# Kernel optimization log

Hardware: AMD Instinct MI355X
Metric: run time of the kernel (lower is better)

Reference implementation:

```python
import jax, jax.numpy as jnp
from jax import lax
import numpy as np

I, H, C = 128, 512, 1000  # input_dim, hidden_dim, num_classes
B, S = 256, 512           # batch, seq_len


def setup_inputs() -> dict:
    key = jax.random.key(0)
    ks = jax.random.split(key, 7)
    k = 1.0 / np.sqrt(H)  # pytorch GRU/Linear init range
    return {
        "x": jax.random.normal(ks[0], (B, S, I), dtype=jnp.float32),
        "W_ih": jax.random.uniform(ks[1], (3 * H, I), minval=-k, maxval=k, dtype=jnp.float32),
        "W_hh": jax.random.uniform(ks[2], (3 * H, H), minval=-k, maxval=k, dtype=jnp.float32),
        "b_ih": jax.random.uniform(ks[3], (3 * H,), minval=-k, maxval=k, dtype=jnp.float32),
        "b_hh": jax.random.uniform(ks[4], (3 * H,), minval=-k, maxval=k, dtype=jnp.float32),
        "W_head": jax.random.uniform(ks[5], (C, H), minval=-k, maxval=k, dtype=jnp.float32),
        "b_head": jax.random.uniform(ks[6], (C,), minval=-k, maxval=k, dtype=jnp.float32),
    }


def reference(x, W_ih, W_hh, b_ih, b_hh, W_head, b_head):
    # Precompute input projections for all timesteps: [B,S,3H] -> [S,B,3H]
    x_gates = jnp.einsum("bsi,gi->bsg", x, W_ih) + b_ih
    x_gates = jnp.transpose(x_gates, (1, 0, 2))

    h0 = jnp.zeros((x.shape[0], W_hh.shape[1]), dtype=x.dtype)

    def step(h, xg):
        hg = h @ W_hh.T + b_hh  # [B,3H]
        xr, xz, xn = jnp.split(xg, 3, axis=-1)
        hr, hz, hn = jnp.split(hg, 3, axis=-1)
        r = jax.nn.sigmoid(xr + hr)
        z = jax.nn.sigmoid(xz + hz)
        n = jnp.tanh(xn + r * hn)
        h_new = (1.0 - z) * n + z * h
        return h_new, None

    hT, _ = lax.scan(step, h0, x_gates)  # final hidden state == outputs[:, -1, :]
    return hT @ W_head.T + b_head  # [B, C]
```

## Files before the change

kernel.cpp:

```cpp
#include <hip/hip_runtime.h>


#define NB 256
#define NH 512
#define NI 128
#define NC 1000
#define NS 512

typedef __attribute__((ext_vector_type(8))) short bf16x8;
typedef __attribute__((ext_vector_type(4))) float f32x4;

__device__ __forceinline__ unsigned short f2bf(float f) {
    unsigned u = __builtin_bit_cast(unsigned, f);
    return (unsigned short)((u + 0x7FFFu + ((u >> 16) & 1u)) >> 16);
}

__device__ __forceinline__ bf16x8 pack8(const float* v) {
    bf16x8 r;
#pragma unroll
    for (int i = 0; i < 8; ++i) r[i] = (short)f2bf(v[i]);
    return r;
}

__device__ __forceinline__ unsigned long long ld_agent_u64(const unsigned long long* p) {
    return __hip_atomic_load(p, __ATOMIC_RELAXED, __HIP_MEMORY_SCOPE_AGENT);
}
__device__ __forceinline__ unsigned int ld_agent_u32(const unsigned int* p) {
    return __hip_atomic_load(p, __ATOMIC_RELAXED, __HIP_MEMORY_SCOPE_AGENT);
}
__device__ __forceinline__ void st_agent_u16(unsigned short* p, unsigned short v) {
    __hip_atomic_store(p, v, __ATOMIC_RELAXED, __HIP_MEMORY_SCOPE_AGENT);
}
__device__ __forceinline__ void st_agent_u32(unsigned int* p, unsigned int v) {
    __hip_atomic_store(p, v, __ATOMIC_RELAXED, __HIP_MEMORY_SCOPE_AGENT);
}

__global__ void gru_init_ws(unsigned int* __restrict__ fl) {
    const int i = blockIdx.x * 256 + threadIdx.x;
    if (i < 512) fl[i] = 0u;
}

__global__ void __launch_bounds__(256, 1) gru_scan(
    const float* __restrict__ x,
    const float* __restrict__ Wih,
    const float* __restrict__ Whh,
    const float* __restrict__ bih,
    const float* __restrict__ bhh,
    unsigned short* __restrict__ hbuf,
    float* __restrict__ hT,
    unsigned int* __restrict__ flags)
{
    const int tid = threadIdx.x;
    const int l   = tid & 63;
    const int w   = tid >> 6;
    const int ch  = w & 1;
    const int kh  = w >> 1;
    const int bid = blockIdx.x;
    const int g   = bid & 15;
    const int jb  = bid >> 4;
    const int r0  = g << 4;
    const int cw0 = (jb << 5) + (ch << 4);
    const int l15 = l & 15;
    const int lq  = l >> 4;
    const int c_col = cw0 + l15;

    __shared__ float part[4][4][64][4];

    bf16x8 whh[3][8];
#pragma unroll
    for (int gt = 0; gt < 3; ++gt) {
        const float* wr = Whh + (size_t)(gt * NH + c_col) * NH;
#pragma unroll
        for (int ks = 0; ks < 8; ++ks) {
            const int k0 = kh * 256 + ks * 32 + lq * 8;
            float tmp[8];
            *(f32x4*)(tmp)     = *(const f32x4*)(wr + k0);
            *(f32x4*)(tmp + 4) = *(const f32x4*)(wr + k0 + 4);
            whh[gt][ks] = pack8(tmp);
        }
    }
    bf16x8 wih[3][2];
#pragma unroll
    for (int gt = 0; gt < 3; ++gt) {
        const float* wr = Wih + (size_t)(gt * NH + c_col) * NI;
#pragma unroll
        for (int ks = 0; ks < 2; ++ks) {
            const int k0 = kh * 64 + ks * 32 + lq * 8;
            float tmp[8];
            *(f32x4*)(tmp)     = *(const f32x4*)(wr + k0);
            *(f32x4*)(tmp + 4) = *(const f32x4*)(wr + k0 + 4);
            wih[gt][ks] = pack8(tmp);
        }
    }

    float bR = bih[c_col] + bhh[c_col];
    float bZ = bih[NH + c_col] + bhh[NH + c_col];
    float bNx = bih[2 * NH + c_col];
    float bNh = bhh[2 * NH + c_col];
    if (kh != 0) { bR = bZ = bNx = bNh = 0.f; }

    float hold0 = 0.f, hold1 = 0.f;

    const float* xptr0 = x + (size_t)(r0 + l15) * (NS * NI) + kh * 64 + lq * 8;
    unsigned int* fl = flags + g * 32;

    const int lanep8 = ((ch * 2 + (l15 >> 3)) * 16 + lq * 4 + kh * 2) * 8;
    const int est    = l15 & 7;

    f32x4 xp0 = *(const f32x4*)(xptr0 + 0);
    f32x4 xp1 = *(const f32x4*)(xptr0 + 4);
    f32x4 xp2 = *(const f32x4*)(xptr0 + 32);
    f32x4 xp3 = *(const f32x4*)(xptr0 + 36);

    for (int t = 0; t < NS; ++t) {
        const int rb = t & 1, wb = rb ^ 1;

        f32x4 aR = {bR, bR, bR, bR}, aZ = {bZ, bZ, bZ, bZ};
        f32x4 aNx = {bNx, bNx, bNx, bNx}, aNh = {bNh, bNh, bNh, bNh};
        {
            float xt[16];
            *(f32x4*)(xt)      = xp0; *(f32x4*)(xt + 4)  = xp1;
            *(f32x4*)(xt + 8)  = xp2; *(f32x4*)(xt + 12) = xp3;
            bf16x8 xf0 = pack8(xt), xf1 = pack8(xt + 8);
            aR  = __builtin_amdgcn_mfma_f32_16x16x32_bf16(xf0, wih[0][0], aR, 0, 0, 0);
            aZ  = __builtin_amdgcn_mfma_f32_16x16x32_bf16(xf0, wih[1][0], aZ, 0, 0, 0);
            aNx = __builtin_amdgcn_mfma_f32_16x16x32_bf16(xf0, wih[2][0], aNx, 0, 0, 0);
            aR  = __builtin_amdgcn_mfma_f32_16x16x32_bf16(xf1, wih[0][1], aR, 0, 0, 0);
            aZ  = __builtin_amdgcn_mfma_f32_16x16x32_bf16(xf1, wih[1][1], aZ, 0, 0, 0);
            aNx = __builtin_amdgcn_mfma_f32_16x16x32_bf16(xf1, wih[2][1], aNx, 0, 0, 0);
        }

        if (t > 0) {
            unsigned int myf;
            do { myf = ld_agent_u32(fl + (l & 15)); }
            while (!__all((int)(myf >= (unsigned)t)));
            __builtin_amdgcn_sched_barrier(0);
            asm volatile("" ::: "memory");

            const unsigned long long* hq =
                (const unsigned long long*)(hbuf + (((size_t)rb * 16 + g) * 16 + kh * 8) * 512);
            bf16x8 afr[8];
#pragma unroll
            for (int f = 0; f < 8; ++f) {
                union { unsigned long long q[2]; bf16x8 v; } u;
                u.q[0] = ld_agent_u64(hq + f * 128 + (l << 1));
                u.q[1] = ld_agent_u64(hq + f * 128 + (l << 1) + 1);
                afr[f] = u.v;
            }

            if (t + 1 < NS) {
                const float* xp = xptr0 + (size_t)(t + 1) * NI;
                xp0 = *(const f32x4*)(xp + 0);
                xp1 = *(const f32x4*)(xp + 4);
                xp2 = *(const f32x4*)(xp + 32);
                xp3 = *(const f32x4*)(xp + 36);
            }

#pragma unroll
            for (int ks = 0; ks < 8; ++ks) {
                aR  = __builtin_amdgcn_mfma_f32_16x16x32_bf16(afr[ks], whh[0][ks], aR, 0, 0, 0);
                aZ  = __builtin_amdgcn_mfma_f32_16x16x32_bf16(afr[ks], whh[1][ks], aZ, 0, 0, 0);
                aNh = __builtin_amdgcn_mfma_f32_16x16x32_bf16(afr[ks], whh[2][ks], aNh, 0, 0, 0);
            }
        } else {
            const float* xp = xptr0 + NI;
            xp0 = *(const f32x4*)(xp + 0);
            xp1 = *(const f32x4*)(xp + 4);
            xp2 = *(const f32x4*)(xp + 32);
            xp3 = *(const f32x4*)(xp + 36);
        }

        *(f32x4*)&part[w][0][l][0] = aR;
        *(f32x4*)&part[w][1][l][0] = aZ;
        *(f32x4*)&part[w][2][l][0] = aNx;
        *(f32x4*)&part[w][3][l][0] = aNh;
        __syncthreads();
        const int pw = w ^ 2;
        const f32x4 pR  = *(const f32x4*)&part[pw][0][l][0];
        const f32x4 pZ  = *(const f32x4*)&part[pw][1][l][0];
        const f32x4 pXn = *(const f32x4*)&part[pw][2][l][0];
        const f32x4 pHn = *(const f32x4*)&part[pw][3][l][0];

        const int i0 = kh * 2;
        float vR[2], vZ[2], vXn[2], vHn[2];
#pragma unroll
        for (int q = 0; q < 2; ++q) {
            vR[q]  = aR[i0 + q]  + pR[i0 + q];
            vZ[q]  = aZ[i0 + q]  + pZ[i0 + q];
            vXn[q] = aNx[i0 + q] + pXn[i0 + q];
            vHn[q] = aNh[i0 + q] + pHn[i0 + q];
        }

        unsigned short* dst = hbuf + (((size_t)wb * 16 + g) * 16 + jb) * 512;
#pragma unroll
        for (int q = 0; q < 2; ++q) {
            const float rr = __builtin_amdgcn_rcpf(1.f + __expf(-vR[q]));
            const float zz = __builtin_amdgcn_rcpf(1.f + __expf(-vZ[q]));
            const float a  = vXn[q] + rr * vHn[q];
            const float e2 = __expf(2.f * a);
            const float nn = (e2 - 1.f) * __builtin_amdgcn_rcpf(e2 + 1.f);
            const float hp = q ? hold1 : hold0;
            const float hnew = (1.f - zz) * nn + zz * hp;
            if (q) hold1 = hnew; else hold0 = hnew;
            if (t < NS - 1) {
                st_agent_u16(dst + lanep8 + q * 8 + est, f2bf(hnew));
            } else {
                hT[(size_t)(r0 + lq * 4 + kh * 2 + q) * NH + c_col] = hnew;
            }
        }

        if (t < NS - 1) {
            asm volatile("s_waitcnt vmcnt(0)" ::: "memory");
            __syncthreads();
            if (tid == 0) st_agent_u32(&fl[jb], (unsigned)(t + 1));
        }
    }
}

__global__ void __launch_bounds__(256, 1) gru_head(
    const float* __restrict__ hT,
    const float* __restrict__ Wh,
    const float* __restrict__ bh,
    float* __restrict__ out)
{
    __shared__ float hs[16 * 512];
    const int tid = threadIdx.x;
    const int rg  = blockIdx.x;
    const int cgp = blockIdx.y;
    const float* src = hT + rg * (16 * 512);
#pragma unroll
    for (int i = 0; i < 32; ++i) hs[tid + 256 * i] = src[tid + 256 * i];
    __syncthreads();
    const int col = (cgp << 6) + (tid & 63);
    const int rb  = (tid >> 6) << 2;
    if (col < NC) {
        const float* wr = Wh + col * NH;
        float a0 = 0.f, a1 = 0.f, a2 = 0.f, a3 = 0.f;
        for (int k = 0; k < NH; k += 4) {
            const f32x4 wv = *(const f32x4*)(wr + k);
            const f32x4 h0 = *(const f32x4*)&hs[(rb + 0) * NH + k];
            const f32x4 h1 = *(const f32x4*)&hs[(rb + 1) * NH + k];
            const f32x4 h2 = *(const f32x4*)&hs[(rb + 2) * NH + k];
            const f32x4 h3 = *(const f32x4*)&hs[(rb + 3) * NH + k];
#pragma unroll
            for (int j = 0; j < 4; ++j) {
                a0 = fmaf(wv[j], h0[j], a0);
                a1 = fmaf(wv[j], h1[j], a1);
                a2 = fmaf(wv[j], h2[j], a2);
                a3 = fmaf(wv[j], h3[j], a3);
            }
        }
        const float bb = bh[col];
        const int orow = (rg << 4) + rb;
        out[(orow + 0) * NC + col] = a0 + bb;
        out[(orow + 1) * NC + col] = a1 + bb;
        out[(orow + 2) * NC + col] = a2 + bb;
        out[(orow + 3) * NC + col] = a3 + bb;
    }
}

extern "C" void kernel_launch(void* const* d_in, const int* in_sizes, int n_in,
                              void* d_out, int out_size, void* d_ws, size_t ws_size,
                              hipStream_t stream)
{
    (void)in_sizes; (void)n_in; (void)out_size; (void)ws_size;
    const float* x     = (const float*)d_in[0];
    const float* Wih   = (const float*)d_in[1];
    const float* Whh   = (const float*)d_in[2];
    const float* bih   = (const float*)d_in[3];
    const float* bhh   = (const float*)d_in[4];
    const float* Whead = (const float*)d_in[5];
    const float* bhead = (const float*)d_in[6];
    float* out = (float*)d_out;

    char* ws = (char*)d_ws;
    unsigned short* hbuf  = (unsigned short*)ws;
    unsigned int*   flags = (unsigned int*)(ws + 512 * 1024);
    float*          hT    = (float*)(ws + 512 * 1024 + 2048);

    gru_init_ws<<<2, 256, 0, stream>>>(flags);
    gru_scan<<<256, 256, 0, stream>>>(x, Wih, Whh, bih, bhh, hbuf, hT, flags);
    gru_head<<<dim3(16, 16), 256, 0, stream>>>(hT, Whead, bhead, out);
}
```

Before: 1.938 ms.

## Transpose MFMA operands, pack hidden-state stores, and overlap input projection before flag wait

Swaps the MFMA operand order so each lane holds four contiguous hidden columns. Only the kh==0 waves run the gate nonlinearity and write the new state as one packed 64-bit store instead of per-element 16-bit stores. The next step's input projection MFMAs now run before the flag publish and the x prefetch moves two steps ahead, so that work falls off the serial critical path. Only wave 0 polls the flags (with s_sleep), and the other waves wait at a block barrier, which adds a __syncthreads per step.

```diff
diff --git a/kernel.cpp b/kernel.cpp
--- a/kernel.cpp
+++ b/kernel.cpp
@@ -28,7 +28,7 @@
 __device__ __forceinline__ unsigned int ld_agent_u32(const unsigned int* p) {
     return __hip_atomic_load(p, __ATOMIC_RELAXED, __HIP_MEMORY_SCOPE_AGENT);
 }
-__device__ __forceinline__ void st_agent_u16(unsigned short* p, unsigned short v) {
+__device__ __forceinline__ void st_agent_u64(unsigned long long* p, unsigned long long v) {
     __hip_atomic_store(p, v, __ATOMIC_RELAXED, __HIP_MEMORY_SCOPE_AGENT);
 }
 __device__ __forceinline__ void st_agent_u32(unsigned int* p, unsigned int v) {
@@ -93,49 +93,64 @@
         }
     }
 
-    float bR = bih[c_col] + bhh[c_col];
-    float bZ = bih[NH + c_col] + bhh[NH + c_col];
-    float bNx = bih[2 * NH + c_col];
-    float bNh = bhh[2 * NH + c_col];
-    if (kh != 0) { bR = bZ = bNx = bNh = 0.f; }
-
-    float hold0 = 0.f, hold1 = 0.f;
+    f32x4 bRv = {0.f,0.f,0.f,0.f}, bZv = bRv, bNxv = bRv, bNhv = bRv;
+    if (kh == 0) {
+#pragma unroll
+        for (int i = 0; i < 4; ++i) {
+            const int col = cw0 + lq * 4 + i;
+            bRv[i]  = bih[col] + bhh[col];
+            bZv[i]  = bih[NH + col] + bhh[NH + col];
+            bNxv[i] = bih[2 * NH + col];
+            bNhv[i] = bhh[2 * NH + col];
+        }
+    }
+
+    float hold[4] = {0.f, 0.f, 0.f, 0.f};
 
     const float* xptr0 = x + (size_t)(r0 + l15) * (NS * NI) + kh * 64 + lq * 8;
     unsigned int* fl = flags + g * 32;
 
-    const int lanep8 = ((ch * 2 + (l15 >> 3)) * 16 + lq * 4 + kh * 2) * 8;
-    const int est    = l15 & 7;
+    const int u64idx = ((2 * ch + (lq >> 1)) * 16 + l15) * 2 + (lq & 1);
 
     f32x4 xp0 = *(const f32x4*)(xptr0 + 0);
     f32x4 xp1 = *(const f32x4*)(xptr0 + 4);
     f32x4 xp2 = *(const f32x4*)(xptr0 + 32);
     f32x4 xp3 = *(const f32x4*)(xptr0 + 36);
 
+    f32x4 aR, aZ, aNx, aNh;
+    {
+        float xt[16];
+        *(f32x4*)(xt)      = xp0; *(f32x4*)(xt + 4)  = xp1;
+        *(f32x4*)(xt + 8)  = xp2; *(f32x4*)(xt + 12) = xp3;
+        bf16x8 xf0 = pack8(xt), xf1 = pack8(xt + 8);
+        aR = bRv; aZ = bZv; aNx = bNxv; aNh = bNhv;
+        aR  = __builtin_amdgcn_mfma_f32_16x16x32_bf16(wih[0][0], xf0, aR, 0, 0, 0);
+        aZ  = __builtin_amdgcn_mfma_f32_16x16x32_bf16(wih[1][0], xf0, aZ, 0, 0, 0);
+        aNx = __builtin_amdgcn_mfma_f32_16x16x32_bf16(wih[2][0], xf0, aNx, 0, 0, 0);
+        aR  = __builtin_amdgcn_mfma_f32_16x16x32_bf16(wih[0][1], xf1, aR, 0, 0, 0);
+        aZ  = __builtin_amdgcn_mfma_f32_16x16x32_bf16(wih[1][1], xf1, aZ, 0, 0, 0);
+        aNx = __builtin_amdgcn_mfma_f32_16x16x32_bf16(wih[2][1], xf1, aNx, 0, 0, 0);
+    }
+    {
+        const float* xp = xptr0 + NI;
+        xp0 = *(const f32x4*)(xp + 0);
+        xp1 = *(const f32x4*)(xp + 4);
+        xp2 = *(const f32x4*)(xp + 32);
+        xp3 = *(const f32x4*)(xp + 36);
+    }
+
     for (int t = 0; t < NS; ++t) {
         const int rb = t & 1, wb = rb ^ 1;
 
-        f32x4 aR = {bR, bR, bR, bR}, aZ = {bZ, bZ, bZ, bZ};
-        f32x4 aNx = {bNx, bNx, bNx, bNx}, aNh = {bNh, bNh, bNh, bNh};
-        {
-            float xt[16];
-            *(f32x4*)(xt)      = xp0; *(f32x4*)(xt + 4)  = xp1;
-            *(f32x4*)(xt + 8)  = xp2; *(f32x4*)(xt + 12) = xp3;
-            bf16x8 xf0 = pack8(xt), xf1 = pack8(xt + 8);
-            aR  = __builtin_amdgcn_mfma_f32_16x16x32_bf16(xf0, wih[0][0], aR, 0, 0, 0);
-            aZ  = __builtin_amdgcn_mfma_f32_16x16x32_bf16(xf0, wih[1][0], aZ, 0, 0, 0);
-            aNx = __builtin_amdgcn_mfma_f32_16x16x32_bf16(xf0, wih[2][0], aNx, 0, 0, 0);
-            aR  = __builtin_amdgcn_mfma_f32_16x16x32_bf16(xf1, wih[0][1], aR, 0, 0, 0);
-            aZ  = __builtin_amdgcn_mfma_f32_16x16x32_bf16(xf1, wih[1][1], aZ, 0, 0, 0);
-            aNx = __builtin_amdgcn_mfma_f32_16x16x32_bf16(xf1, wih[2][1], aNx, 0, 0, 0);
-        }
-
         if (t > 0) {
-            unsigned int myf;
-            do { myf = ld_agent_u32(fl + (l & 15)); }
-            while (!__all((int)(myf >= (unsigned)t)));
-            __builtin_amdgcn_sched_barrier(0);
-            asm volatile("" ::: "memory");
+            if (w == 0) {
+                unsigned int myf = ld_agent_u32(fl + l15);
+                while (!__all((int)(myf >= (unsigned)t))) {
+                    __builtin_amdgcn_s_sleep(1);
+                    myf = ld_agent_u32(fl + (l & 15));
+                }
+            }
+            __syncthreads();
 
             const unsigned long long* hq =
                 (const unsigned long long*)(hbuf + (((size_t)rb * 16 + g) * 16 + kh * 8) * 512);
@@ -147,27 +162,12 @@
                 u.q[1] = ld_agent_u64(hq + f * 128 + (l << 1) + 1);
                 afr[f] = u.v;
             }
-
-            if (t + 1 < NS) {
-                const float* xp = xptr0 + (size_t)(t + 1) * NI;
-                xp0 = *(const f32x4*)(xp + 0);
-                xp1 = *(const f32x4*)(xp + 4);
-                xp2 = *(const f32x4*)(xp + 32);
-                xp3 = *(const f32x4*)(xp + 36);
-            }
-
 #pragma unroll
             for (int ks = 0; ks < 8; ++ks) {
-                aR  = __builtin_amdgcn_mfma_f32_16x16x32_bf16(afr[ks], whh[0][ks], aR, 0, 0, 0);
-                aZ  = __builtin_amdgcn_mfma_f32_16x16x32_bf16(afr[ks], whh[1][ks], aZ, 0, 0, 0);
-                aNh = __builtin_amdgcn_mfma_f32_16x16x32_bf16(afr[ks], whh[2][ks], aNh, 0, 0, 0);
-            }
-        } else {
-            const float* xp = xptr0 + NI;
-            xp0 = *(const f32x4*)(xp + 0);
-            xp1 = *(const f32x4*)(xp + 4);
-            xp2 = *(const f32x4*)(xp + 32);
-            xp3 = *(const f32x4*)(xp + 36);
+                aR  = __builtin_amdgcn_mfma_f32_16x16x32_bf16(whh[0][ks], afr[ks], aR, 0, 0, 0);
+                aZ  = __builtin_amdgcn_mfma_f32_16x16x32_bf16(whh[1][ks], afr[ks], aZ, 0, 0, 0);
+                aNh = __builtin_amdgcn_mfma_f32_16x16x32_bf16(whh[2][ks], afr[ks], aNh, 0, 0, 0);
+            }
         }
 
         *(f32x4*)&part[w][0][l][0] = aR;
@@ -175,44 +175,68 @@
         *(f32x4*)&part[w][2][l][0] = aNx;
         *(f32x4*)&part[w][3][l][0] = aNh;
         __syncthreads();
-        const int pw = w ^ 2;
-        const f32x4 pR  = *(const f32x4*)&part[pw][0][l][0];
-        const f32x4 pZ  = *(const f32x4*)&part[pw][1][l][0];
-        const f32x4 pXn = *(const f32x4*)&part[pw][2][l][0];
-        const f32x4 pHn = *(const f32x4*)&part[pw][3][l][0];
-
-        const int i0 = kh * 2;
-        float vR[2], vZ[2], vXn[2], vHn[2];
-#pragma unroll
-        for (int q = 0; q < 2; ++q) {
-            vR[q]  = aR[i0 + q]  + pR[i0 + q];
-            vZ[q]  = aZ[i0 + q]  + pZ[i0 + q];
-            vXn[q] = aNx[i0 + q] + pXn[i0 + q];
-            vHn[q] = aNh[i0 + q] + pHn[i0 + q];
-        }
-
-        unsigned short* dst = hbuf + (((size_t)wb * 16 + g) * 16 + jb) * 512;
-#pragma unroll
-        for (int q = 0; q < 2; ++q) {
-            const float rr = __builtin_amdgcn_rcpf(1.f + __expf(-vR[q]));
-            const float zz = __builtin_amdgcn_rcpf(1.f + __expf(-vZ[q]));
-            const float a  = vXn[q] + rr * vHn[q];
-            const float e2 = __expf(2.f * a);
-            const float nn = (e2 - 1.f) * __builtin_amdgcn_rcpf(e2 + 1.f);
-            const float hp = q ? hold1 : hold0;
-            const float hnew = (1.f - zz) * nn + zz * hp;
-            if (q) hold1 = hnew; else hold0 = hnew;
+
+        if (kh == 0) {
+            const int pw = w ^ 2;
+            const f32x4 pR  = *(const f32x4*)&part[pw][0][l][0];
+            const f32x4 pZ  = *(const f32x4*)&part[pw][1][l][0];
+            const f32x4 pXn = *(const f32x4*)&part[pw][2][l][0];
+            const f32x4 pHn = *(const f32x4*)&part[pw][3][l][0];
+
+            float hnew[4];
+#pragma unroll
+            for (int i = 0; i < 4; ++i) {
+                const float vR  = aR[i]  + pR[i];
+                const float vZ  = aZ[i]  + pZ[i];
+                const float vXn = aNx[i] + pXn[i];
+                const float vHn = aNh[i] + pHn[i];
+                const float rr = __builtin_amdgcn_rcpf(1.f + __expf(-vR));
+                const float zz = __builtin_amdgcn_rcpf(1.f + __expf(-vZ));
+                const float a  = vXn + rr * vHn;
+                const float e2 = __expf(2.f * a);
+                const float nn = (e2 - 1.f) * __builtin_amdgcn_rcpf(e2 + 1.f);
+                hnew[i] = (1.f - zz) * nn + zz * hold[i];
+                hold[i] = hnew[i];
+            }
+
             if (t < NS - 1) {
-                st_agent_u16(dst + lanep8 + q * 8 + est, f2bf(hnew));
+                unsigned long long pk =
+                      (unsigned long long)f2bf(hnew[0])
+                    | ((unsigned long long)f2bf(hnew[1]) << 16)
+                    | ((unsigned long long)f2bf(hnew[2]) << 32)
+                    | ((unsigned long long)f2bf(hnew[3]) << 48);
+                unsigned long long* dst =
+                    (unsigned long long*)(hbuf + (((size_t)wb * 16 + g) * 16 + jb) * 512);
+                st_agent_u64(dst + u64idx, pk);
             } else {
-                hT[(size_t)(r0 + lq * 4 + kh * 2 + q) * NH + c_col] = hnew;
+                *(f32x4*)&hT[(size_t)(r0 + l15) * NH + cw0 + lq * 4] = *(f32x4*)hnew;
             }
         }
 
         if (t < NS - 1) {
+            float xt[16];
+            *(f32x4*)(xt)      = xp0; *(f32x4*)(xt + 4)  = xp1;
+            *(f32x4*)(xt + 8)  = xp2; *(f32x4*)(xt + 12) = xp3;
+            bf16x8 xf0 = pack8(xt), xf1 = pack8(xt + 8);
+            aR = bRv; aZ = bZv; aNx = bNxv; aNh = bNhv;
+            aR  = __builtin_amdgcn_mfma_f32_16x16x32_bf16(wih[0][0], xf0, aR, 0, 0, 0);
+            aZ  = __builtin_amdgcn_mfma_f32_16x16x32_bf16(wih[1][0], xf0, aZ, 0, 0, 0);
+            aNx = __builtin_amdgcn_mfma_f32_16x16x32_bf16(wih[2][0], xf0, aNx, 0, 0, 0);
+            aR  = __builtin_amdgcn_mfma_f32_16x16x32_bf16(wih[0][1], xf1, aR, 0, 0, 0);
+            aZ  = __builtin_amdgcn_mfma_f32_16x16x32_bf16(wih[1][1], xf1, aZ, 0, 0, 0);
+            aNx = __builtin_amdgcn_mfma_f32_16x16x32_bf16(wih[2][1], xf1, aNx, 0, 0, 0);
+
             asm volatile("s_waitcnt vmcnt(0)" ::: "memory");
             __syncthreads();
             if (tid == 0) st_agent_u32(&fl[jb], (unsigned)(t + 1));
+
+            if (t + 2 < NS) {
+                const float* xp = xptr0 + (size_t)(t + 2) * NI;
+                xp0 = *(const f32x4*)(xp + 0);
+                xp1 = *(const f32x4*)(xp + 4);
+                xp2 = *(const f32x4*)(xp + 32);
+                xp3 = *(const f32x4*)(xp + 36);
+            }
         }
     }
 }
```

Result: faster. 1.700 ms (-12.3%).
